# Optimization experiments

Measured on AMD Instinct MI355X. Metric: run time of the kernel, lower is better.

The kernel has to match this reference:

```python
import jax, jax.numpy as jnp
import numpy as np

N = 500_000      # nodes
B = 8192         # graphs
F = 128          # num_node_features
C = 128          # channels (num_out_features)
EPS = 1e-16      # matches torch_geometric.utils.softmax denominator eps


def setup_inputs() -> dict:
    key = jax.random.key(0)
    ks = jax.random.split(key, 16)
    w = lambda k, shape: jax.random.normal(k, shape, dtype=jnp.float32) * 0.02
    inp = {
        "x": jax.random.normal(ks[0], (N, F), dtype=jnp.float32),
        "u": jax.random.normal(ks[1], (B, C), dtype=jnp.float32),
        "batch": jnp.sort(jax.random.randint(ks[2], (N,), 0, B, dtype=jnp.int32)),
        "size": B,
        # gate_nn: Linear(C,C) -> ReLU -> Linear(C,1)
        "gate_w1": w(ks[3], (C, C)), "gate_b1": w(ks[4], (C,)),
        "gate_w2": w(ks[5], (C, 1)), "gate_b2": w(ks[6], (1,)),
        # node_nn: Linear(F,C) -> ReLU -> Linear(C,C)
        "node_w1": w(ks[7], (F, C)), "node_b1": w(ks[8], (C,)),
        "node_w2": w(ks[9], (C, C)), "node_b2": w(ks[10], (C,)),
        # ques_nn: Linear(C,C) -> ReLU -> Linear(C,C)
        "ques_w1": w(ks[11], (C, C)), "ques_b1": w(ks[12], (C,)),
        "ques_w2": w(ks[13], (C, C)), "ques_b2": w(ks[14], (C,)),
    }
    return inp


def _mlp2(x, w1, b1, w2, b2):
    return jax.nn.relu(x @ w1 + b1) @ w2 + b2


def reference(x, u, batch, size,
              gate_w1, gate_b1, gate_w2, gate_b2,
              node_w1, node_b1, node_w2, node_b2,
              ques_w1, ques_b1, ques_w2, ques_b2):
    # node features h_theta(x): [N, C]
    h = _mlp2(x, node_w1, node_b1, node_w2, node_b2)
    # question features per graph, gathered to nodes: [N, C]
    q = _mlp2(u, ques_w1, ques_b1, ques_w2, ques_b2)
    # gate scores: [N, 1]
    gate = _mlp2(q[batch] * h, gate_w1, gate_b1, gate_w2, gate_b2)
    # segment softmax over graphs (torch_geometric.utils.softmax)
    m = jax.ops.segment_max(gate, batch, num_segments=size)          # [B, 1]
    m = jnp.where(jnp.isfinite(m), m, 0.0)                            # empty segments
    e = jnp.exp(gate - m[batch])                                      # [N, 1]
    s = jax.ops.segment_sum(e, batch, num_segments=size)              # [B, 1]
    alpha = e / (s[batch] + EPS)                                      # [N, 1]
    # scatter_add pooling: [B, C]
    out = jax.ops.segment_sum(alpha * h, batch, num_segments=size)
    return out
```

## Files before the change

### kernel.cpp

```cpp
#include <hip/hip_runtime.h>
#include <math.h>

#define NN 500000
#define NB 8192
#define GMAX 16
#define TILE_M 128

typedef _Float16 f16x8 __attribute__((ext_vector_type(8)));
typedef float f32x4 __attribute__((ext_vector_type(4)));

__device__ inline f16x8 zero8() {
    f16x8 v;
#pragma unroll
    for (int i = 0; i < 8; ++i) v[i] = (_Float16)0.f;
    return v;
}

__global__ void prep_w(const float* __restrict__ nw1, const float* __restrict__ nw2,
                       const float* __restrict__ gw1, const float* __restrict__ gw2,
                       const float* __restrict__ qw1, const float* __restrict__ qw2,
                       _Float16* __restrict__ wT1, _Float16* __restrict__ wT2,
                       _Float16* __restrict__ wTg, _Float16* __restrict__ wTq1,
                       _Float16* __restrict__ wTq2, _Float16* __restrict__ g2h) {
    int k = blockIdx.x;
    int n = threadIdx.x;
    wT1[n * 128 + k]  = (_Float16)nw1[k * 128 + n];
    wT2[n * 128 + k]  = (_Float16)nw2[k * 128 + n];
    wTg[n * 128 + k]  = (_Float16)gw1[k * 128 + n];
    wTq1[n * 128 + k] = (_Float16)qw1[k * 128 + n];
    wTq2[n * 128 + k] = (_Float16)qw2[k * 128 + n];
    if (k == 0) g2h[n] = (_Float16)gw2[n];
}

__launch_bounds__(512, 4)
__global__ void q_kernel(const float* __restrict__ u,
                         const _Float16* __restrict__ wTq1, const _Float16* __restrict__ wTq2,
                         const float* __restrict__ qb1, const float* __restrict__ qb2,
                         _Float16* __restrict__ q, float* __restrict__ P, float* __restrict__ s) {
    __shared__ __align__(16) _Float16 tbuf[TILE_M][136];
    const int tid  = threadIdx.x;
    const int wave = tid >> 6;
    const int lane = tid & 63;
    const int lrow = lane & 15;
    const int quad = lane >> 4;
    const int wr   = wave >> 1;
    const int wc   = wave & 1;
    const int row0 = blockIdx.x * TILE_M;
    const int rbase = wr * 32;

    for (int idx = tid; idx < TILE_M * 128; idx += 512) P[(size_t)row0 * 128 + idx] = 0.f;
    if (tid < TILE_M) s[row0 + tid] = 0.f;

    f32x4 acc[2][4];
    const f32x4 fz = {0.f, 0.f, 0.f, 0.f};
#pragma unroll
    for (int mi = 0; mi < 2; ++mi)
#pragma unroll
        for (int ci = 0; ci < 4; ++ci) acc[mi][ci] = fz;

#pragma unroll
    for (int ki = 0; ki < 4; ++ki) {
        const int k = ki * 32 + quad * 8;
        f16x8 a[2];
#pragma unroll
        for (int mi = 0; mi < 2; ++mi) {
            int r = row0 + rbase + mi * 16 + lrow;
            const float4* up = (const float4*)(u + (size_t)r * 128 + k);
            float4 x0 = up[0], x1 = up[1];
            f16x8 af;
            af[0] = (_Float16)x0.x; af[1] = (_Float16)x0.y;
            af[2] = (_Float16)x0.z; af[3] = (_Float16)x0.w;
            af[4] = (_Float16)x1.x; af[5] = (_Float16)x1.y;
            af[6] = (_Float16)x1.z; af[7] = (_Float16)x1.w;
            a[mi] = af;
        }
        f16x8 b[4];
#pragma unroll
        for (int ci = 0; ci < 4; ++ci)
            b[ci] = *(const f16x8*)(wTq1 + (size_t)(wc * 64 + ci * 16 + lrow) * 128 + k);
#pragma unroll
        for (int mi = 0; mi < 2; ++mi)
#pragma unroll
            for (int ci = 0; ci < 4; ++ci)
                acc[mi][ci] = __builtin_amdgcn_mfma_f32_16x16x32_f16(a[mi], b[ci], acc[mi][ci], 0, 0, 0);
    }
#pragma unroll
    for (int ci = 0; ci < 4; ++ci) {
        int c = wc * 64 + ci * 16 + lrow;
        float bv = qb1[c];
#pragma unroll
        for (int mi = 0; mi < 2; ++mi)
#pragma unroll
            for (int i = 0; i < 4; ++i) {
                int r = rbase + mi * 16 + quad * 4 + i;
                tbuf[r][c] = (_Float16)fmaxf(acc[mi][ci][i] + bv, 0.f);
            }
    }
    __syncthreads();

#pragma unroll
    for (int mi = 0; mi < 2; ++mi)
#pragma unroll
        for (int ci = 0; ci < 4; ++ci) acc[mi][ci] = fz;
#pragma unroll
    for (int ki = 0; ki < 4; ++ki) {
        const int k = ki * 32 + quad * 8;
        f16x8 a[2];
#pragma unroll
        for (int mi = 0; mi < 2; ++mi)
            a[mi] = *(const f16x8*)&tbuf[rbase + mi * 16 + lrow][k];
        f16x8 b[4];
#pragma unroll
        for (int ci = 0; ci < 4; ++ci)
            b[ci] = *(const f16x8*)(wTq2 + (size_t)(wc * 64 + ci * 16 + lrow) * 128 + k);
#pragma unroll
        for (int mi = 0; mi < 2; ++mi)
#pragma unroll
            for (int ci = 0; ci < 4; ++ci)
                acc[mi][ci] = __builtin_amdgcn_mfma_f32_16x16x32_f16(a[mi], b[ci], acc[mi][ci], 0, 0, 0);
    }
#pragma unroll
    for (int ci = 0; ci < 4; ++ci) {
        int c = wc * 64 + ci * 16 + lrow;
        float bv = qb2[c];
#pragma unroll
        for (int mi = 0; mi < 2; ++mi)
#pragma unroll
            for (int i = 0; i < 4; ++i) {
                int r = row0 + rbase + mi * 16 + quad * 4 + i;
                q[(size_t)r * 128 + c] = (_Float16)(acc[mi][ci][i] + bv);
            }
    }
}

__launch_bounds__(512, 4)
__global__ void hg_kernel(const float* __restrict__ x, const int* __restrict__ batch,
                          const _Float16* __restrict__ qglob,
                          const _Float16* __restrict__ wT1, const _Float16* __restrict__ wT2,
                          const _Float16* __restrict__ wTg, const _Float16* __restrict__ g2h,
                          const float* __restrict__ nb1, const float* __restrict__ nb2,
                          const float* __restrict__ gb1, const float* __restrict__ gb2,
                          float* __restrict__ P, float* __restrict__ s) {
    __shared__ __align__(16) _Float16 tbuf[TILE_M][136];
    __shared__ float qs[GMAX][132];
    __shared__ __align__(16) _Float16 E_sh[GMAX][136];
    __shared__ int batch_t[TILE_M];
    __shared__ int maxrel_sh;

    const int tid  = threadIdx.x;
    const int wave = tid >> 6;
    const int lane = tid & 63;
    const int lrow = lane & 15;
    const int quad = lane >> 4;
    const int wr   = wave >> 1;
    const int wc   = wave & 1;
    const int row0 = blockIdx.x * TILE_M;
    const int rbase = wr * 32;

    if (tid < TILE_M) {
        int gr = row0 + tid;
        batch_t[tid] = (gr < NN) ? batch[gr] : batch[NN - 1];
    }
    if (tid == 0) maxrel_sh = 0;
    for (int idx = tid; idx < GMAX * 136 / 2; idx += 512) ((float*)E_sh)[idx] = 0.f;
    __syncthreads();
    const int b_lo = batch_t[0];
    if (tid < TILE_M) atomicMax(&maxrel_sh, batch_t[tid] - b_lo);
    __syncthreads();
    const int maxrel = maxrel_sh;
    const int gcnt = min(maxrel + 1, GMAX);
    for (int idx = tid; idx < gcnt * 128; idx += 512) {
        int g = idx >> 7, c = idx & 127;
        qs[g][c] = (float)qglob[(size_t)(b_lo + g) * 128 + c];
    }
    __syncthreads();

    f32x4 acc[2][4];
    const f32x4 fz = {0.f, 0.f, 0.f, 0.f};
#pragma unroll
    for (int mi = 0; mi < 2; ++mi)
#pragma unroll
        for (int ci = 0; ci < 4; ++ci) acc[mi][ci] = fz;

#pragma unroll
    for (int ki = 0; ki < 4; ++ki) {
        const int k = ki * 32 + quad * 8;
        f16x8 a[2];
#pragma unroll
        for (int mi = 0; mi < 2; ++mi) {
            int r = row0 + rbase + mi * 16 + lrow;
            if (r < NN) {
                const float4* xp = (const float4*)(x + (size_t)r * 128 + k);
                float4 x0 = xp[0], x1 = xp[1];
                f16x8 af;
                af[0] = (_Float16)x0.x; af[1] = (_Float16)x0.y;
                af[2] = (_Float16)x0.z; af[3] = (_Float16)x0.w;
                af[4] = (_Float16)x1.x; af[5] = (_Float16)x1.y;
                af[6] = (_Float16)x1.z; af[7] = (_Float16)x1.w;
                a[mi] = af;
            } else {
                a[mi] = zero8();
            }
        }
        f16x8 b[4];
#pragma unroll
        for (int ci = 0; ci < 4; ++ci)
            b[ci] = *(const f16x8*)(wT1 + (size_t)(wc * 64 + ci * 16 + lrow) * 128 + k);
#pragma unroll
        for (int mi = 0; mi < 2; ++mi)
#pragma unroll
            for (int ci = 0; ci < 4; ++ci)
                acc[mi][ci] = __builtin_amdgcn_mfma_f32_16x16x32_f16(a[mi], b[ci], acc[mi][ci], 0, 0, 0);
    }
#pragma unroll
    for (int ci = 0; ci < 4; ++ci) {
        int c = wc * 64 + ci * 16 + lrow;
        float bv = nb1[c];
#pragma unroll
        for (int mi = 0; mi < 2; ++mi)
#pragma unroll
            for (int i = 0; i < 4; ++i) {
                int r = rbase + mi * 16 + quad * 4 + i;
                tbuf[r][c] = (_Float16)fmaxf(acc[mi][ci][i] + bv, 0.f);
            }
    }
    __syncthreads();

#pragma unroll
    for (int mi = 0; mi < 2; ++mi)
#pragma unroll
        for (int ci = 0; ci < 4; ++ci) acc[mi][ci] = fz;
#pragma unroll
    for (int ki = 0; ki < 4; ++ki) {
        const int k = ki * 32 + quad * 8;
        f16x8 a[2];
#pragma unroll
        for (int mi = 0; mi < 2; ++mi)
            a[mi] = *(const f16x8*)&tbuf[rbase + mi * 16 + lrow][k];
        f16x8 b[4];
#pragma unroll
        for (int ci = 0; ci < 4; ++ci)
            b[ci] = *(const f16x8*)(wT2 + (size_t)(wc * 64 + ci * 16 + lrow) * 128 + k);
#pragma unroll
        for (int mi = 0; mi < 2; ++mi)
#pragma unroll
            for (int ci = 0; ci < 4; ++ci)
                acc[mi][ci] = __builtin_amdgcn_mfma_f32_16x16x32_f16(a[mi], b[ci], acc[mi][ci], 0, 0, 0);
    }
    f32x4 hreg[2][4];
    int grel[2][4];
#pragma unroll
    for (int mi = 0; mi < 2; ++mi)
#pragma unroll
        for (int i = 0; i < 4; ++i) {
            int r = rbase + mi * 16 + quad * 4 + i;
            grel[mi][i] = batch_t[r] - b_lo;
        }
#pragma unroll
    for (int ci = 0; ci < 4; ++ci) {
        int c = wc * 64 + ci * 16 + lrow;
        float bv = nb2[c];
#pragma unroll
        for (int mi = 0; mi < 2; ++mi)
#pragma unroll
            for (int i = 0; i < 4; ++i) {
                float h = acc[mi][ci][i] + bv;
                hreg[mi][ci][i] = h;
                int g = grel[mi][i];
                float qv = (g < GMAX) ? qs[g][c]
                                      : (float)qglob[(size_t)(b_lo + g) * 128 + c];
                acc[mi][ci][i] = qv * h;
            }
    }
    __syncthreads();
#pragma unroll
    for (int ci = 0; ci < 4; ++ci) {
        int c = wc * 64 + ci * 16 + lrow;
#pragma unroll
        for (int mi = 0; mi < 2; ++mi)
#pragma unroll
            for (int i = 0; i < 4; ++i) {
                int r = rbase + mi * 16 + quad * 4 + i;
                tbuf[r][c] = (_Float16)acc[mi][ci][i];
            }
    }
    __syncthreads();

#pragma unroll
    for (int mi = 0; mi < 2; ++mi)
#pragma unroll
        for (int ci = 0; ci < 4; ++ci) acc[mi][ci] = fz;
#pragma unroll
    for (int ki = 0; ki < 4; ++ki) {
        const int k = ki * 32 + quad * 8;
        f16x8 a[2];
#pragma unroll
        for (int mi = 0; mi < 2; ++mi)
            a[mi] = *(const f16x8*)&tbuf[rbase + mi * 16 + lrow][k];
        f16x8 b[4];
#pragma unroll
        for (int ci = 0; ci < 4; ++ci)
            b[ci] = *(const f16x8*)(wTg + (size_t)(wc * 64 + ci * 16 + lrow) * 128 + k);
#pragma unroll
        for (int mi = 0; mi < 2; ++mi)
#pragma unroll
            for (int ci = 0; ci < 4; ++ci)
                acc[mi][ci] = __builtin_amdgcn_mfma_f32_16x16x32_f16(a[mi], b[ci], acc[mi][ci], 0, 0, 0);
    }
#pragma unroll
    for (int ci = 0; ci < 4; ++ci) {
        int c = wc * 64 + ci * 16 + lrow;
        float bv = gb1[c];
#pragma unroll
        for (int mi = 0; mi < 2; ++mi)
#pragma unroll
            for (int i = 0; i < 4; ++i)
                acc[mi][ci][i] = fmaxf(acc[mi][ci][i] + bv, 0.f);
    }
    __syncthreads();
#pragma unroll
    for (int ci = 0; ci < 4; ++ci) {
        int c = wc * 64 + ci * 16 + lrow;
#pragma unroll
        for (int mi = 0; mi < 2; ++mi)
#pragma unroll
            for (int i = 0; i < 4; ++i) {
                int r = rbase + mi * 16 + quad * 4 + i;
                tbuf[r][c] = (_Float16)acc[mi][ci][i];
            }
    }
    __syncthreads();

    f32x4 gacc[2];
    gacc[0] = fz; gacc[1] = fz;
#pragma unroll
    for (int ki = 0; ki < 4; ++ki) {
        const int k = ki * 32 + quad * 8;
        f16x8 bg = *(const f16x8*)(g2h + k);
#pragma unroll
        for (int mi = 0; mi < 2; ++mi) {
            f16x8 a = *(const f16x8*)&tbuf[rbase + mi * 16 + lrow][k];
            gacc[mi] = __builtin_amdgcn_mfma_f32_16x16x32_f16(a, bg, gacc[mi], 0, 0, 0);
        }
    }
    const float gb2v = gb2[0];

#pragma unroll
    for (int mi = 0; mi < 2; ++mi)
#pragma unroll
        for (int i = 0; i < 4; ++i) {
            int r = rbase + mi * 16 + quad * 4 + i;
            bool valid = (row0 + r) < NN;
            float e = valid ? expf(gacc[mi][i] + gb2v) : 0.f;
            int g = grel[mi][i];
            if (g < GMAX) {
                if (wc == 0 && lrow == 0) E_sh[g][r] = (_Float16)e;
            } else {
                if (wc == 0 && lrow == 0) atomicAdd(&s[b_lo + g], e);
#pragma unroll
                for (int ci = 0; ci < 4; ++ci) {
                    int c = wc * 64 + ci * 16 + lrow;
                    atomicAdd(&P[(size_t)(b_lo + g) * 128 + c], e * hreg[mi][ci][i]);
                }
            }
        }
    __syncthreads();

#pragma unroll
    for (int ci = 0; ci < 4; ++ci) {
        int c = wc * 64 + ci * 16 + lrow;
#pragma unroll
        for (int mi = 0; mi < 2; ++mi)
#pragma unroll
            for (int i = 0; i < 4; ++i) {
                int r = rbase + mi * 16 + quad * 4 + i;
                tbuf[c][r] = (_Float16)hreg[mi][ci][i];
            }
    }
    __syncthreads();

    f32x4 pacc = fz;
    f32x4 spool = fz;
    f16x8 bO;
#pragma unroll
    for (int j = 0; j < 8; ++j) bO[j] = (lrow == 0) ? (_Float16)1.f : (_Float16)0.f;
#pragma unroll
    for (int ki = 0; ki < 4; ++ki) {
        const int k = ki * 32 + quad * 8;
        f16x8 aE = *(const f16x8*)&E_sh[lrow][k];
        f16x8 bH = *(const f16x8*)&tbuf[wave * 16 + lrow][k];
        pacc = __builtin_amdgcn_mfma_f32_16x16x32_f16(aE, bH, pacc, 0, 0, 0);
        if (wave == 0)
            spool = __builtin_amdgcn_mfma_f32_16x16x32_f16(aE, bO, spool, 0, 0, 0);
    }
#pragma unroll
    for (int i = 0; i < 4; ++i) {
        int g = quad * 4 + i;
        if (g < gcnt)
            atomicAdd(&P[(size_t)(b_lo + g) * 128 + wave * 16 + lrow], pacc[i]);
    }
    if (wave == 0 && lrow == 0) {
#pragma unroll
        for (int i = 0; i < 4; ++i) {
            int g = quad * 4 + i;
            if (g < gcnt) atomicAdd(&s[b_lo + g], spool[i]);
        }
    }
}

__global__ void fin_kernel(float* __restrict__ P, const float* __restrict__ s) {
    int idx = blockIdx.x * 256 + threadIdx.x;
    if (idx < NB * 128) P[idx] = P[idx] / (s[idx >> 7] + 1e-16f);
}

extern "C" void kernel_launch(void* const* d_in, const int* in_sizes, int n_in,
                              void* d_out, int out_size, void* d_ws, size_t ws_size,
                              hipStream_t stream) {
    const float* x    = (const float*)d_in[0];
    const float* u    = (const float*)d_in[1];
    const int* batch  = (const int*)d_in[2];
    const float* gw1  = (const float*)d_in[4];
    const float* gb1  = (const float*)d_in[5];
    const float* gw2  = (const float*)d_in[6];
    const float* gb2  = (const float*)d_in[7];
    const float* nw1  = (const float*)d_in[8];
    const float* nb1  = (const float*)d_in[9];
    const float* nw2  = (const float*)d_in[10];
    const float* nb2  = (const float*)d_in[11];
    const float* qw1  = (const float*)d_in[12];
    const float* qb1  = (const float*)d_in[13];
    const float* qw2  = (const float*)d_in[14];
    const float* qb2  = (const float*)d_in[15];

    char* ws = (char*)d_ws;
    _Float16* q = (_Float16*)ws;
    float* s = (float*)(ws + 2097152);
    _Float16* wT1 = (_Float16*)(ws + 2129920);
    _Float16* wT2  = wT1 + 16384;
    _Float16* wTg  = wT2 + 16384;
    _Float16* wTq1 = wTg + 16384;
    _Float16* wTq2 = wTq1 + 16384;
    _Float16* g2h  = wTq2 + 16384;
    float* P = (float*)d_out;

    hipLaunchKernelGGL(prep_w, dim3(128), dim3(128), 0, stream,
                       nw1, nw2, gw1, gw2, qw1, qw2, wT1, wT2, wTg, wTq1, wTq2, g2h);
    hipLaunchKernelGGL(q_kernel, dim3(NB / TILE_M), dim3(512), 0, stream,
                       u, wTq1, wTq2, qb1, qb2, q, P, s);
    hipLaunchKernelGGL(hg_kernel, dim3((NN + TILE_M - 1) / TILE_M), dim3(512), 0, stream,
                       x, batch, q, wT1, wT2, wTg, g2h, nb1, nb2, gb1, gb2, P, s);
    hipLaunchKernelGGL(fin_kernel, dim3((NB * 128 + 255) / 256), dim3(256), 0, stream, P, s);
}
```

Before: 622.8 us.

## Pool pre-activation node features and apply second node layer after segment pooling

Uses linearity of the second node-MLP layer to pool alpha-weighted ReLU(x W1 + b1) per graph, then applies W2 and the bias (scaled by the segment sum) once per graph in the final kernel. This removes the transpose of h in the pooling stage. The gate's final Linear(C,1) becomes a register dot product with shuffle reductions instead of an extra LDS round-trip and MFMA. The hg kernel moves to 64-row tiles with 256 threads, prefetches x up front, and uses packed cvt_pkrtz conversions. The changes add a workspace buffer for pre-pooling sums and a small GEMM in the finish kernel, and rounding may differ slightly since the pooled sums are cast to fp16 before the W2 matmul.

After: 557.0 us. -10.6%, faster.

```diff
diff --git a/kernel.cpp b/kernel.cpp
--- a/kernel.cpp
+++ b/kernel.cpp
@@ -4,16 +4,18 @@
 #define NN 500000
 #define NB 8192
 #define GMAX 16
-#define TILE_M 128
 
 typedef _Float16 f16x8 __attribute__((ext_vector_type(8)));
+typedef __fp16 fp16x2 __attribute__((ext_vector_type(2)));
 typedef float f32x4 __attribute__((ext_vector_type(4)));
 
-__device__ inline f16x8 zero8() {
-    f16x8 v;
-#pragma unroll
-    for (int i = 0; i < 8; ++i) v[i] = (_Float16)0.f;
-    return v;
+__device__ inline f16x8 cvt8(float4 a, float4 b) {
+    union { fp16x2 p[4]; f16x8 r; } u;
+    u.p[0] = __builtin_amdgcn_cvt_pkrtz(a.x, a.y);
+    u.p[1] = __builtin_amdgcn_cvt_pkrtz(a.z, a.w);
+    u.p[2] = __builtin_amdgcn_cvt_pkrtz(b.x, b.y);
+    u.p[3] = __builtin_amdgcn_cvt_pkrtz(b.z, b.w);
+    return u.r;
 }
 
 __global__ void prep_w(const float* __restrict__ nw1, const float* __restrict__ nw2,
@@ -36,8 +38,8 @@
 __global__ void q_kernel(const float* __restrict__ u,
                          const _Float16* __restrict__ wTq1, const _Float16* __restrict__ wTq2,
                          const float* __restrict__ qb1, const float* __restrict__ qb2,
-                         _Float16* __restrict__ q, float* __restrict__ P, float* __restrict__ s) {
-    __shared__ __align__(16) _Float16 tbuf[TILE_M][136];
+                         _Float16* __restrict__ q, float* __restrict__ Ppre, float* __restrict__ s) {
+    __shared__ __align__(16) _Float16 tbuf[128][136];
     const int tid  = threadIdx.x;
     const int wave = tid >> 6;
     const int lane = tid & 63;
@@ -45,11 +47,11 @@
     const int quad = lane >> 4;
     const int wr   = wave >> 1;
     const int wc   = wave & 1;
-    const int row0 = blockIdx.x * TILE_M;
+    const int row0 = blockIdx.x * 128;
     const int rbase = wr * 32;
 
-    for (int idx = tid; idx < TILE_M * 128; idx += 512) P[(size_t)row0 * 128 + idx] = 0.f;
-    if (tid < TILE_M) s[row0 + tid] = 0.f;
+    for (int idx = tid; idx < 128 * 128; idx += 512) Ppre[(size_t)row0 * 128 + idx] = 0.f;
+    if (tid < 128) s[row0 + tid] = 0.f;
 
     f32x4 acc[2][4];
     const f32x4 fz = {0.f, 0.f, 0.f, 0.f};
@@ -66,13 +68,7 @@
         for (int mi = 0; mi < 2; ++mi) {
             int r = row0 + rbase + mi * 16 + lrow;
             const float4* up = (const float4*)(u + (size_t)r * 128 + k);
-            float4 x0 = up[0], x1 = up[1];
-            f16x8 af;
-            af[0] = (_Float16)x0.x; af[1] = (_Float16)x0.y;
-            af[2] = (_Float16)x0.z; af[3] = (_Float16)x0.w;
-            af[4] = (_Float16)x1.x; af[5] = (_Float16)x1.y;
-            af[6] = (_Float16)x1.z; af[7] = (_Float16)x1.w;
-            a[mi] = af;
+            a[mi] = cvt8(up[0], up[1]);
         }
         f16x8 b[4];
 #pragma unroll
@@ -133,18 +129,20 @@
     }
 }
 
-__launch_bounds__(512, 4)
+__launch_bounds__(256, 4)
 __global__ void hg_kernel(const float* __restrict__ x, const int* __restrict__ batch,
                           const _Float16* __restrict__ qglob,
                           const _Float16* __restrict__ wT1, const _Float16* __restrict__ wT2,
                           const _Float16* __restrict__ wTg, const _Float16* __restrict__ g2h,
                           const float* __restrict__ nb1, const float* __restrict__ nb2,
                           const float* __restrict__ gb1, const float* __restrict__ gb2,
-                          float* __restrict__ P, float* __restrict__ s) {
-    __shared__ __align__(16) _Float16 tbuf[TILE_M][136];
-    __shared__ float qs[GMAX][132];
-    __shared__ __align__(16) _Float16 E_sh[GMAX][136];
-    __shared__ int batch_t[TILE_M];
+                          float* __restrict__ Ppre, float* __restrict__ s) {
+    __shared__ __align__(16) _Float16 t1buf[64][136];
+    __shared__ __align__(16) _Float16 scratch[64][136];
+    __shared__ __align__(16) _Float16 qsE[GMAX][136];
+    __shared__ float gpart[2][64];
+    __shared__ float sacc[GMAX];
+    __shared__ int batch_t[64];
     __shared__ int maxrel_sh;
 
     const int tid  = threadIdx.x;
@@ -154,26 +152,50 @@
     const int quad = lane >> 4;
     const int wr   = wave >> 1;
     const int wc   = wave & 1;
-    const int row0 = blockIdx.x * TILE_M;
+    const int row0 = blockIdx.x * 64;
     const int rbase = wr * 32;
 
-    if (tid < TILE_M) {
-        int gr = row0 + tid;
-        batch_t[tid] = (gr < NN) ? batch[gr] : batch[NN - 1];
-    }
-    if (tid == 0) maxrel_sh = 0;
-    for (int idx = tid; idx < GMAX * 136 / 2; idx += 512) ((float*)E_sh)[idx] = 0.f;
+    float4 xraw[4][2][2];
+#pragma unroll
+    for (int ki = 0; ki < 4; ++ki)
+#pragma unroll
+        for (int mi = 0; mi < 2; ++mi) {
+            int r = min(row0 + rbase + mi * 16 + lrow, NN - 1);
+            const float4* xp = (const float4*)(x + (size_t)r * 128 + ki * 32 + quad * 8);
+            xraw[ki][mi][0] = xp[0];
+            xraw[ki][mi][1] = xp[1];
+        }
+
+    if (wave == 0) {
+        int bv = batch[min(row0 + lane, NN - 1)];
+        batch_t[lane] = bv;
+        int b0 = __shfl(bv, 0, 64);
+        int rel = bv - b0;
+#pragma unroll
+        for (int off = 32; off >= 1; off >>= 1) rel = max(rel, __shfl_xor(rel, off, 64));
+        if (lane == 0) maxrel_sh = rel;
+    }
     __syncthreads();
     const int b_lo = batch_t[0];
-    if (tid < TILE_M) atomicMax(&maxrel_sh, batch_t[tid] - b_lo);
-    __syncthreads();
-    const int maxrel = maxrel_sh;
-    const int gcnt = min(maxrel + 1, GMAX);
-    for (int idx = tid; idx < gcnt * 128; idx += 512) {
-        int g = idx >> 7, c = idx & 127;
-        qs[g][c] = (float)qglob[(size_t)(b_lo + g) * 128 + c];
-    }
-    __syncthreads();
+    const int gcnt = min(maxrel_sh + 1, GMAX);
+
+    for (int idx = tid; idx < gcnt * 16; idx += 256)
+        *(f16x8*)&qsE[idx >> 4][(idx & 15) * 8] =
+            *(const f16x8*)(qglob + (size_t)(b_lo + (idx >> 4)) * 128 + (idx & 15) * 8);
+
+    int grel[2][4];
+#pragma unroll
+    for (int mi = 0; mi < 2; ++mi)
+#pragma unroll
+        for (int i = 0; i < 4; ++i)
+            grel[mi][i] = batch_t[rbase + mi * 16 + quad * 4 + i] - b_lo;
+
+    f16x8 a16[4][2];
+#pragma unroll
+    for (int ki = 0; ki < 4; ++ki)
+#pragma unroll
+        for (int mi = 0; mi < 2; ++mi)
+            a16[ki][mi] = cvt8(xraw[ki][mi][0], xraw[ki][mi][1]);
 
     f32x4 acc[2][4];
     const f32x4 fz = {0.f, 0.f, 0.f, 0.f};
@@ -185,232 +207,229 @@
 #pragma unroll
     for (int ki = 0; ki < 4; ++ki) {
         const int k = ki * 32 + quad * 8;
+        f16x8 b[4];
+#pragma unroll
+        for (int ci = 0; ci < 4; ++ci)
+            b[ci] = *(const f16x8*)(wT1 + (size_t)(wc * 64 + ci * 16 + lrow) * 128 + k);
+#pragma unroll
+        for (int mi = 0; mi < 2; ++mi)
+#pragma unroll
+            for (int ci = 0; ci < 4; ++ci)
+                acc[mi][ci] = __builtin_amdgcn_mfma_f32_16x16x32_f16(a16[ki][mi], b[ci], acc[mi][ci], 0, 0, 0);
+    }
+#pragma unroll
+    for (int ci = 0; ci < 4; ++ci) {
+        int c = wc * 64 + ci * 16 + lrow;
+        float bv = nb1[c];
+#pragma unroll
+        for (int mi = 0; mi < 2; ++mi)
+#pragma unroll
+            for (int i = 0; i < 4; ++i) {
+                int r = rbase + mi * 16 + quad * 4 + i;
+                t1buf[r][c] = (_Float16)fmaxf(acc[mi][ci][i] + bv, 0.f);
+            }
+    }
+    __syncthreads();
+
+#pragma unroll
+    for (int mi = 0; mi < 2; ++mi)
+#pragma unroll
+        for (int ci = 0; ci < 4; ++ci) acc[mi][ci] = fz;
+#pragma unroll
+    for (int ki = 0; ki < 4; ++ki) {
+        const int k = ki * 32 + quad * 8;
+        f16x8 a[2];
+#pragma unroll
+        for (int mi = 0; mi < 2; ++mi)
+            a[mi] = *(const f16x8*)&t1buf[rbase + mi * 16 + lrow][k];
+        f16x8 b[4];
+#pragma unroll
+        for (int ci = 0; ci < 4; ++ci)
+            b[ci] = *(const f16x8*)(wT2 + (size_t)(wc * 64 + ci * 16 + lrow) * 128 + k);
+#pragma unroll
+        for (int mi = 0; mi < 2; ++mi)
+#pragma unroll
+            for (int ci = 0; ci < 4; ++ci)
+                acc[mi][ci] = __builtin_amdgcn_mfma_f32_16x16x32_f16(a[mi], b[ci], acc[mi][ci], 0, 0, 0);
+    }
+#pragma unroll
+    for (int ci = 0; ci < 4; ++ci) {
+        int c = wc * 64 + ci * 16 + lrow;
+        float bv = nb2[c];
+#pragma unroll
+        for (int mi = 0; mi < 2; ++mi)
+#pragma unroll
+            for (int i = 0; i < 4; ++i) {
+                int r = rbase + mi * 16 + quad * 4 + i;
+                float h = acc[mi][ci][i] + bv;
+                int g = grel[mi][i];
+                float qv = (g < GMAX) ? (float)qsE[g][c]
+                                      : (float)qglob[(size_t)(b_lo + g) * 128 + c];
+                scratch[r][c] = (_Float16)(qv * h);
+            }
+    }
+    __syncthreads();
+
+    for (int idx = tid; idx < GMAX * 136 / 2; idx += 256) ((float*)qsE)[idx] = 0.f;
+    if (tid < GMAX) sacc[tid] = 0.f;
+
+#pragma unroll
+    for (int mi = 0; mi < 2; ++mi)
+#pragma unroll
+        for (int ci = 0; ci < 4; ++ci) acc[mi][ci] = fz;
+    float g2hreg[4];
+#pragma unroll
+    for (int ci = 0; ci < 4; ++ci) g2hreg[ci] = (float)g2h[wc * 64 + ci * 16 + lrow];
+#pragma unroll
+    for (int ki = 0; ki < 4; ++ki) {
+        const int k = ki * 32 + quad * 8;
+        f16x8 a[2];
+#pragma unroll
+        for (int mi = 0; mi < 2; ++mi)
+            a[mi] = *(const f16x8*)&scratch[rbase + mi * 16 + lrow][k];
+        f16x8 b[4];
+#pragma unroll
+        for (int ci = 0; ci < 4; ++ci)
+            b[ci] = *(const f16x8*)(wTg + (size_t)(wc * 64 + ci * 16 + lrow) * 128 + k);
+#pragma unroll
+        for (int mi = 0; mi < 2; ++mi)
+#pragma unroll
+            for (int ci = 0; ci < 4; ++ci)
+                acc[mi][ci] = __builtin_amdgcn_mfma_f32_16x16x32_f16(a[mi], b[ci], acc[mi][ci], 0, 0, 0);
+    }
+    float p[2][4] = {{0.f, 0.f, 0.f, 0.f}, {0.f, 0.f, 0.f, 0.f}};
+#pragma unroll
+    for (int ci = 0; ci < 4; ++ci) {
+        int c = wc * 64 + ci * 16 + lrow;
+        float bv = gb1[c];
+        float w = g2hreg[ci];
+#pragma unroll
+        for (int mi = 0; mi < 2; ++mi)
+#pragma unroll
+            for (int i = 0; i < 4; ++i)
+                p[mi][i] = fmaf(fmaxf(acc[mi][ci][i] + bv, 0.f), w, p[mi][i]);
+    }
+#pragma unroll
+    for (int off = 1; off <= 8; off <<= 1)
+#pragma unroll
+        for (int mi = 0; mi < 2; ++mi)
+#pragma unroll
+            for (int i = 0; i < 4; ++i)
+                p[mi][i] += __shfl_xor(p[mi][i], off, 64);
+    if (lrow == 0) {
+#pragma unroll
+        for (int mi = 0; mi < 2; ++mi)
+#pragma unroll
+            for (int i = 0; i < 4; ++i)
+                gpart[wc][rbase + mi * 16 + quad * 4 + i] = p[mi][i];
+    }
+    __syncthreads();
+
+    const float gb2v = gb2[0];
+    if (tid < 64) {
+        int r = tid;
+        int g = batch_t[r] - b_lo;
+        bool valid = (row0 + r) < NN;
+        float e = valid ? __expf(gpart[0][r] + gpart[1][r] + gb2v) : 0.f;
+        if (g < GMAX) {
+            qsE[g][r] = (_Float16)e;
+            atomicAdd(&sacc[g], e);
+        } else if (valid) {
+            atomicAdd(&s[b_lo + g], e);
+            for (int c = 0; c < 128; ++c)
+                atomicAdd(&Ppre[(size_t)(b_lo + g) * 128 + c], e * (float)t1buf[r][c]);
+        }
+    }
+    __syncthreads();
+
+    f16x8 aE[2];
+#pragma unroll
+    for (int ki = 0; ki < 2; ++ki)
+        aE[ki] = *(const f16x8*)&qsE[lrow][ki * 32 + quad * 8];
+    f32x4 pacc[2] = {fz, fz};
+#pragma unroll
+    for (int ci2 = 0; ci2 < 2; ++ci2) {
+        int col = wave * 32 + ci2 * 16 + lrow;
+#pragma unroll
+        for (int ki = 0; ki < 2; ++ki) {
+            f16x8 bh;
+#pragma unroll
+            for (int j = 0; j < 8; ++j) bh[j] = t1buf[ki * 32 + quad * 8 + j][col];
+            pacc[ci2] = __builtin_amdgcn_mfma_f32_16x16x32_f16(aE[ki], bh, pacc[ci2], 0, 0, 0);
+        }
+    }
+#pragma unroll
+    for (int ci2 = 0; ci2 < 2; ++ci2)
+#pragma unroll
+        for (int i = 0; i < 4; ++i) {
+            int g = quad * 4 + i;
+            if (g < gcnt)
+                atomicAdd(&Ppre[(size_t)(b_lo + g) * 128 + wave * 32 + ci2 * 16 + lrow], pacc[ci2][i]);
+        }
+    if (tid < gcnt) atomicAdd(&s[b_lo + tid], sacc[tid]);
+}
+
+__launch_bounds__(512, 4)
+__global__ void fin_kernel(const float* __restrict__ Ppre, const float* __restrict__ s,
+                           const _Float16* __restrict__ wT2, const float* __restrict__ nb2,
+                           float* __restrict__ out) {
+    const int tid  = threadIdx.x;
+    const int wave = tid >> 6;
+    const int lane = tid & 63;
+    const int lrow = lane & 15;
+    const int quad = lane >> 4;
+    const int wr   = wave >> 1;
+    const int wc   = wave & 1;
+    const int row0 = blockIdx.x * 128;
+    const int rbase = wr * 32;
+
+    f32x4 acc[2][4];
+    const f32x4 fz = {0.f, 0.f, 0.f, 0.f};
+#pragma unroll
+    for (int mi = 0; mi < 2; ++mi)
+#pragma unroll
+        for (int ci = 0; ci < 4; ++ci) acc[mi][ci] = fz;
+#pragma unroll
+    for (int ki = 0; ki < 4; ++ki) {
+        const int k = ki * 32 + quad * 8;
         f16x8 a[2];
 #pragma unroll
         for (int mi = 0; mi < 2; ++mi) {
             int r = row0 + rbase + mi * 16 + lrow;
-            if (r < NN) {
-                const float4* xp = (const float4*)(x + (size_t)r * 128 + k);
-                float4 x0 = xp[0], x1 = xp[1];
-                f16x8 af;
-                af[0] = (_Float16)x0.x; af[1] = (_Float16)x0.y;
-                af[2] = (_Float16)x0.z; af[3] = (_Float16)x0.w;
-                af[4] = (_Float16)x1.x; af[5] = (_Float16)x1.y;
-                af[6] = (_Float16)x1.z; af[7] = (_Float16)x1.w;
-                a[mi] = af;
-            } else {
-                a[mi] = zero8();
+            const float4* pp = (const float4*)(Ppre + (size_t)r * 128 + k);
+            a[mi] = cvt8(pp[0], pp[1]);
+        }
+        f16x8 b[4];
+#pragma unroll
+        for (int ci = 0; ci < 4; ++ci)
+            b[ci] = *(const f16x8*)(wT2 + (size_t)(wc * 64 + ci * 16 + lrow) * 128 + k);
+#pragma unroll
+        for (int mi = 0; mi < 2; ++mi)
+#pragma unroll
+            for (int ci = 0; ci < 4; ++ci)
+                acc[mi][ci] = __builtin_amdgcn_mfma_f32_16x16x32_f16(a[mi], b[ci], acc[mi][ci], 0, 0, 0);
+    }
+    float sv[2][4], rinv[2][4];
+#pragma unroll
+    for (int mi = 0; mi < 2; ++mi)
+#pragma unroll
+        for (int i = 0; i < 4; ++i) {
+            int r = row0 + rbase + mi * 16 + quad * 4 + i;
+            sv[mi][i] = s[r];
+            rinv[mi][i] = 1.f / (sv[mi][i] + 1e-16f);
+        }
+#pragma unroll
+    for (int ci = 0; ci < 4; ++ci) {
+        int c = wc * 64 + ci * 16 + lrow;
+        float bv = nb2[c];
+#pragma unroll
+        for (int mi = 0; mi < 2; ++mi)
+#pragma unroll
+            for (int i = 0; i < 4; ++i) {
+                int r = row0 + rbase + mi * 16 + quad * 4 + i;
+                out[(size_t)r * 128 + c] = (acc[mi][ci][i] + sv[mi][i] * bv) * rinv[mi][i];
             }
-        }
-        f16x8 b[4];
-#pragma unroll
-        for (int ci = 0; ci < 4; ++ci)
-            b[ci] = *(const f16x8*)(wT1 + (size_t)(wc * 64 + ci * 16 + lrow) * 128 + k);
-#pragma unroll
-        for (int mi = 0; mi < 2; ++mi)
-#pragma unroll
-            for (int ci = 0; ci < 4; ++ci)
-                acc[mi][ci] = __builtin_amdgcn_mfma_f32_16x16x32_f16(a[mi], b[ci], acc[mi][ci], 0, 0, 0);
-    }
-#pragma unroll
-    for (int ci = 0; ci < 4; ++ci) {
-        int c = wc * 64 + ci * 16 + lrow;
-        float bv = nb1[c];
-#pragma unroll
-        for (int mi = 0; mi < 2; ++mi)
-#pragma unroll
-            for (int i = 0; i < 4; ++i) {
-                int r = rbase + mi * 16 + quad * 4 + i;
-                tbuf[r][c] = (_Float16)fmaxf(acc[mi][ci][i] + bv, 0.f);
-            }
-    }
-    __syncthreads();
-
-#pragma unroll
-    for (int mi = 0; mi < 2; ++mi)
-#pragma unroll
-        for (int ci = 0; ci < 4; ++ci) acc[mi][ci] = fz;
-#pragma unroll
-    for (int ki = 0; ki < 4; ++ki) {
-        const int k = ki * 32 + quad * 8;
-        f16x8 a[2];
-#pragma unroll
-        for (int mi = 0; mi < 2; ++mi)
-            a[mi] = *(const f16x8*)&tbuf[rbase + mi * 16 + lrow][k];
-        f16x8 b[4];
-#pragma unroll
-        for (int ci = 0; ci < 4; ++ci)
-            b[ci] = *(const f16x8*)(wT2 + (size_t)(wc * 64 + ci * 16 + lrow) * 128 + k);
-#pragma unroll
-        for (int mi = 0; mi < 2; ++mi)
-#pragma unroll
-            for (int ci = 0; ci < 4; ++ci)
-                acc[mi][ci] = __builtin_amdgcn_mfma_f32_16x16x32_f16(a[mi], b[ci], acc[mi][ci], 0, 0, 0);
-    }
-    f32x4 hreg[2][4];
-    int grel[2][4];
-#pragma unroll
-    for (int mi = 0; mi < 2; ++mi)
-#pragma unroll
-        for (int i = 0; i < 4; ++i) {
-            int r = rbase + mi * 16 + quad * 4 + i;
-            grel[mi][i] = batch_t[r] - b_lo;
-        }
-#pragma unroll
-    for (int ci = 0; ci < 4; ++ci) {
-        int c = wc * 64 + ci * 16 + lrow;
-        float bv = nb2[c];
-#pragma unroll
-        for (int mi = 0; mi < 2; ++mi)
-#pragma unroll
-            for (int i = 0; i < 4; ++i) {
-                float h = acc[mi][ci][i] + bv;
-                hreg[mi][ci][i] = h;
-                int g = grel[mi][i];
-                float qv = (g < GMAX) ? qs[g][c]
-                                      : (float)qglob[(size_t)(b_lo + g) * 128 + c];
-                acc[mi][ci][i] = qv * h;
-            }
-    }
-    __syncthreads();
-#pragma unroll
-    for (int ci = 0; ci < 4; ++ci) {
-        int c = wc * 64 + ci * 16 + lrow;
-#pragma unroll
-        for (int mi = 0; mi < 2; ++mi)
-#pragma unroll
-            for (int i = 0; i < 4; ++i) {
-                int r = rbase + mi * 16 + quad * 4 + i;
-                tbuf[r][c] = (_Float16)acc[mi][ci][i];
-            }
-    }
-    __syncthreads();
-
-#pragma unroll
-    for (int mi = 0; mi < 2; ++mi)
-#pragma unroll
-        for (int ci = 0; ci < 4; ++ci) acc[mi][ci] = fz;
-#pragma unroll
-    for (int ki = 0; ki < 4; ++ki) {
-        const int k = ki * 32 + quad * 8;
-        f16x8 a[2];
-#pragma unroll
-        for (int mi = 0; mi < 2; ++mi)
-            a[mi] = *(const f16x8*)&tbuf[rbase + mi * 16 + lrow][k];
-        f16x8 b[4];
-#pragma unroll
-        for (int ci = 0; ci < 4; ++ci)
-            b[ci] = *(const f16x8*)(wTg + (size_t)(wc * 64 + ci * 16 + lrow) * 128 + k);
-#pragma unroll
-        for (int mi = 0; mi < 2; ++mi)
-#pragma unroll
-            for (int ci = 0; ci < 4; ++ci)
-                acc[mi][ci] = __builtin_amdgcn_mfma_f32_16x16x32_f16(a[mi], b[ci], acc[mi][ci], 0, 0, 0);
-    }
-#pragma unroll
-    for (int ci = 0; ci < 4; ++ci) {
-        int c = wc * 64 + ci * 16 + lrow;
-        float bv = gb1[c];
-#pragma unroll
-        for (int mi = 0; mi < 2; ++mi)
-#pragma unroll
-            for (int i = 0; i < 4; ++i)
-                acc[mi][ci][i] = fmaxf(acc[mi][ci][i] + bv, 0.f);
-    }
-    __syncthreads();
-#pragma unroll
-    for (int ci = 0; ci < 4; ++ci) {
-        int c = wc * 64 + ci * 16 + lrow;
-#pragma unroll
-        for (int mi = 0; mi < 2; ++mi)
-#pragma unroll
-            for (int i = 0; i < 4; ++i) {
-                int r = rbase + mi * 16 + quad * 4 + i;
-                tbuf[r][c] = (_Float16)acc[mi][ci][i];
-            }
-    }
-    __syncthreads();
-
-    f32x4 gacc[2];
-    gacc[0] = fz; gacc[1] = fz;
-#pragma unroll
-    for (int ki = 0; ki < 4; ++ki) {
-        const int k = ki * 32 + quad * 8;
-        f16x8 bg = *(const f16x8*)(g2h + k);
-#pragma unroll
-        for (int mi = 0; mi < 2; ++mi) {
-            f16x8 a = *(const f16x8*)&tbuf[rbase + mi * 16 + lrow][k];
-            gacc[mi] = __builtin_amdgcn_mfma_f32_16x16x32_f16(a, bg, gacc[mi], 0, 0, 0);
-        }
-    }
-    const float gb2v = gb2[0];
-
-#pragma unroll
-    for (int mi = 0; mi < 2; ++mi)
-#pragma unroll
-        for (int i = 0; i < 4; ++i) {
-            int r = rbase + mi * 16 + quad * 4 + i;
-            bool valid = (row0 + r) < NN;
-            float e = valid ? expf(gacc[mi][i] + gb2v) : 0.f;
-            int g = grel[mi][i];
-            if (g < GMAX) {
-                if (wc == 0 && lrow == 0) E_sh[g][r] = (_Float16)e;
-            } else {
-                if (wc == 0 && lrow == 0) atomicAdd(&s[b_lo + g], e);
-#pragma unroll
-                for (int ci = 0; ci < 4; ++ci) {
-                    int c = wc * 64 + ci * 16 + lrow;
-                    atomicAdd(&P[(size_t)(b_lo + g) * 128 + c], e * hreg[mi][ci][i]);
-                }
-            }
-        }
-    __syncthreads();
-
-#pragma unroll
-    for (int ci = 0; ci < 4; ++ci) {
-        int c = wc * 64 + ci * 16 + lrow;
-#pragma unroll
-        for (int mi = 0; mi < 2; ++mi)
-#pragma unroll
-            for (int i = 0; i < 4; ++i) {
-                int r = rbase + mi * 16 + quad * 4 + i;
-                tbuf[c][r] = (_Float16)hreg[mi][ci][i];
-            }
-    }
-    __syncthreads();
-
-    f32x4 pacc = fz;
-    f32x4 spool = fz;
-    f16x8 bO;
-#pragma unroll
-    for (int j = 0; j < 8; ++j) bO[j] = (lrow == 0) ? (_Float16)1.f : (_Float16)0.f;
-#pragma unroll
-    for (int ki = 0; ki < 4; ++ki) {
-        const int k = ki * 32 + quad * 8;
-        f16x8 aE = *(const f16x8*)&E_sh[lrow][k];
-        f16x8 bH = *(const f16x8*)&tbuf[wave * 16 + lrow][k];
-        pacc = __builtin_amdgcn_mfma_f32_16x16x32_f16(aE, bH, pacc, 0, 0, 0);
-        if (wave == 0)
-            spool = __builtin_amdgcn_mfma_f32_16x16x32_f16(aE, bO, spool, 0, 0, 0);
-    }
-#pragma unroll
-    for (int i = 0; i < 4; ++i) {
-        int g = quad * 4 + i;
-        if (g < gcnt)
-            atomicAdd(&P[(size_t)(b_lo + g) * 128 + wave * 16 + lrow], pacc[i]);
-    }
-    if (wave == 0 && lrow == 0) {
-#pragma unroll
-        for (int i = 0; i < 4; ++i) {
-            int g = quad * 4 + i;
-            if (g < gcnt) atomicAdd(&s[b_lo + g], spool[i]);
-        }
-    }
-}
-
-__global__ void fin_kernel(float* __restrict__ P, const float* __restrict__ s) {
-    int idx = blockIdx.x * 256 + threadIdx.x;
-    if (idx < NB * 128) P[idx] = P[idx] / (s[idx >> 7] + 1e-16f);
+    }
 }
 
 extern "C" void kernel_launch(void* const* d_in, const int* in_sizes, int n_in,
@@ -433,21 +452,23 @@
     const float* qb2  = (const float*)d_in[15];
 
     char* ws = (char*)d_ws;
-    _Float16* q = (_Float16*)ws;
-    float* s = (float*)(ws + 2097152);
-    _Float16* wT1 = (_Float16*)(ws + 2129920);
+    _Float16* q   = (_Float16*)ws;
+    float* Ppre   = (float*)(ws + 2097152);
+    float* s      = (float*)(ws + 6291456);
+    _Float16* wT1 = (_Float16*)(ws + 6324224);
     _Float16* wT2  = wT1 + 16384;
     _Float16* wTg  = wT2 + 16384;
     _Float16* wTq1 = wTg + 16384;
     _Float16* wTq2 = wTq1 + 16384;
     _Float16* g2h  = wTq2 + 16384;
-    float* P = (float*)d_out;
+    float* out = (float*)d_out;
 
     hipLaunchKernelGGL(prep_w, dim3(128), dim3(128), 0, stream,
                        nw1, nw2, gw1, gw2, qw1, qw2, wT1, wT2, wTg, wTq1, wTq2, g2h);
-    hipLaunchKernelGGL(q_kernel, dim3(NB / TILE_M), dim3(512), 0, stream,
-                       u, wTq1, wTq2, qb1, qb2, q, P, s);
-    hipLaunchKernelGGL(hg_kernel, dim3((NN + TILE_M - 1) / TILE_M), dim3(512), 0, stream,
-                       x, batch, q, wT1, wT2, wTg, g2h, nb1, nb2, gb1, gb2, P, s);
-    hipLaunchKernelGGL(fin_kernel, dim3((NB * 128 + 255) / 256), dim3(256), 0, stream, P, s);
-}
+    hipLaunchKernelGGL(q_kernel, dim3(NB / 128), dim3(512), 0, stream,
+                       u, wTq1, wTq2, qb1, qb2, q, Ppre, s);
+    hipLaunchKernelGGL(hg_kernel, dim3((NN + 63) / 64), dim3(256), 0, stream,
+                       x, batch, q, wT1, wT2, wTg, g2h, nb1, nb2, gb1, gb2, Ppre, s);
+    hipLaunchKernelGGL(fin_kernel, dim3(NB / 128), dim3(512), 0, stream,
+                       Ppre, s, wT2, nb2, out);
+}
```
